# Kernel optimization log

Measured on AMD Instinct MI355X. Metric: run time of the kernel, lower is better.

The kernel has to match this reference:

```python
import jax, jax.numpy as jnp
import numpy as np

S, B, H, V = 64, 8, 512, 8192  # seq_length, batch, hidden, vocab
NEG = -1e9  # finite stand-in for -inf so gradients stay clean


def setup_inputs() -> dict:
    key = jax.random.key(0)
    ks = jax.random.split(key, 8)
    lin = lambda k, fi, fo: jax.random.normal(k, (fi, fo), jnp.float32) * 0.05
    return dict(
        h=jax.random.normal(ks[0], (S, B, H), jnp.float32) * 0.1,
        sentence=jax.random.randint(ks[1], (S, B), 0, V),
        t_W1=lin(ks[2], 2 * H, H), t_b1=jnp.zeros((H,), jnp.float32),
        t_W2=lin(ks[3], H, 1), t_b2=jnp.zeros((1,), jnp.float32),
        w_W1=lin(ks[4], 2 * H, H), w_b1=jnp.zeros((H,), jnp.float32),
        w_W2=lin(ks[5], H, V), w_b2=jnp.zeros((V,), jnp.float32),
    )


def _inside(h, sentence, t_W1, t_b1, t_W2, t_b2, w_W1, w_b1, w_W2, w_b2):
    sent_length = S - 1
    # ---- transition scores on full (i, j) grid: concat(h_i, h_j) -> MLP -> scalar
    hi = jnp.broadcast_to(h[:, None], (S, S, B, H))
    hj = jnp.broadcast_to(h[None, :], (S, S, B, H))
    feat = jnp.concatenate([hi, hj], axis=-1)                      # [S,S,B,2H]
    t = (jax.nn.relu(feat @ t_W1 + t_b1) @ t_W2 + t_b2)[..., 0]    # [S,S,B]
    sh_lp = jax.nn.log_sigmoid(-t)   # log p(shift | i, j)
    re_lp = jax.nn.log_sigmoid(t)    # log p(reduce | i, j)

    # ---- word generation log-probs for pairs (i, j), i < j <= sent_length-1
    iu, ju = jnp.triu_indices(sent_length, k=1)                    # P pairs
    hp = jnp.concatenate([h[iu], h[ju]], axis=-1)                  # [P,B,2H]
    logits = jax.nn.relu(hp @ w_W1 + w_b1) @ w_W2 + w_b2           # [P,B,V]
    lse = jax.scipy.special.logsumexp(logits, axis=-1)             # [P,B]
    tok = sentence[ju + 1]                                         # [P,B]
    tok_logit = jnp.take_along_axis(logits, tok[..., None], axis=-1)[..., 0]
    word_lp = tok_logit - lse
    # shift prob + word prob (word_prob_list in the original)
    wp = jnp.full((S, S, B), NEG, jnp.float32).at[iu, ju].set(sh_lp[iu, ju] + word_lp)

    # ---- DP table init
    table = jnp.full((S, S, B), NEG, jnp.float32)
    f0 = jnp.concatenate([h[0], h[0]], axis=-1)                    # [B,2H]
    lg0 = jax.nn.relu(f0 @ w_W1 + w_b1) @ w_W2 + w_b2              # [B,V]
    init_lp = jnp.take_along_axis(jax.nn.log_softmax(lg0, axis=-1),
                                  sentence[1][:, None], axis=1)[:, 0]
    table = table.at[0, 1].set(init_lp)
    jd = jnp.arange(1, sent_length)
    table = table.at[jd, jd + 1].set(0.0)

    # ---- diagonal sweep: table[i,j] = LSE_k( table[i,k]+table[k,j]+wp[i,k]+re[k,j] )
    ivec = jnp.arange(S)
    mvec = jnp.arange(1, S)

    def step(tab, g):
        i = ivec[:, None]
        m = mvec[None, :]
        k = jnp.clip(i + m, 0, S - 1)                              # [S,S-1]
        jv = jnp.clip(ivec + g, 0, S - 1)                          # [S]
        j = jv[:, None]
        valid = (m < g) & (ivec[:, None] + g <= sent_length)       # [S,S-1]
        sc = tab[i, k] + tab[k, j] + wp[i, k] + re_lp[k, j]        # [S,S-1,B]
        sc = jnp.where(valid[..., None], sc, NEG)
        mmax = jnp.max(sc, axis=1, keepdims=True)
        new = jnp.log(jnp.sum(jnp.exp(sc - mmax), axis=1)) + mmax[:, 0]
        row_ok = (ivec + g <= sent_length)[:, None]
        tab = tab.at[ivec, jv].set(jnp.where(row_ok, new, tab[ivec, jv]))
        return tab, None

    table, _ = jax.lax.scan(step, table, jnp.arange(2, sent_length + 1))
    final = table[0, sent_length] + re_lp[0, sent_length]          # [B]
    return -jnp.sum(final)  # neg_log_likelihood


def reference(h, sentence, t_W1, t_b1, t_W2, t_b2, w_W1, w_b1, w_W2, w_b2):
    return _inside(h, sentence, t_W1, t_b1, t_W2, t_b2, w_W1, w_b1, w_W2, w_b2)
```

## Files before the change

kernel.cpp:

```cpp
#include <hip/hip_runtime.h>
#include <hip/hip_bf16.h>
#include <hip/hip_fp8.h>
#include <math.h>

#define NEG (-1.0e9f)

typedef __bf16 bf16_t;
typedef __bf16 bf16x4 __attribute__((ext_vector_type(4)));
typedef __bf16 bf16x8 __attribute__((ext_vector_type(8)));
typedef float f32x4 __attribute__((ext_vector_type(4)));
typedef long i64x2 __attribute__((ext_vector_type(2)));
typedef unsigned char u8;
typedef unsigned long long u64;

#define SS 64
#define BB 8
#define HH 512
#define VV 8192
#define NPAIR 1953
#define NPTOT 1954
#define MROWS (NPTOT*BB)
#define MPAD  16384

__device__ __forceinline__ float logsig(float x) {
  return fminf(x, 0.f) - __logf(1.f + __expf(-fabsf(x)));
}
__device__ __forceinline__ u8 f2q(float x) { __hip_fp8_e4m3 q(x); return q.__x; }
__device__ __forceinline__ float q2f(u8 b) { __hip_fp8_e4m3 q; q.__x = b; return (float)q; }
__device__ __forceinline__ int ksl(int c) { return 2 * (c & 3) + (c >> 2); }

__global__ __launch_bounds__(256) void k_prep(
    const float* __restrict__ h,   bf16_t* __restrict__ hbf,
    const float* __restrict__ tW1, bf16_t* __restrict__ tW1T,
    const float* __restrict__ wW1, bf16_t* __restrict__ wW1T,
    const float* __restrict__ wW2, u8* __restrict__ w2t8) {
  __shared__ float tile[32][33];
  int blk = blockIdx.x, tid = threadIdx.x;
  if (blk < 256) {
    int gi = blk * 256 + tid;
    float4 v = ((const float4*)h)[gi];
    bf16x4 o = {(bf16_t)v.x, (bf16_t)v.y, (bf16_t)v.z, (bf16_t)v.w};
    ((bf16x4*)hbf)[gi] = o;
    return;
  }
  if (blk < 1280) {
    const float* in; bf16_t* out; int R = 1024, C = 512, t;
    if (blk < 768) { in = tW1; out = tW1T; t = blk - 256; }
    else           { in = wW1; out = wW1T; t = blk - 768; }
    int xt = C / 32;
    int c0 = (t % xt) * 32, r0 = (t / xt) * 32;
    int tx = tid & 31, ty = tid >> 5;
    for (int i = ty; i < 32; i += 8)
      tile[i][tx] = in[(size_t)(r0 + i) * C + c0 + tx];
    __syncthreads();
    for (int i = ty; i < 32; i += 8)
      out[(size_t)(c0 + i) * R + r0 + tx] = (bf16_t)tile[tx][i];
    return;
  }
  int t = blk - 1280;
  int c0 = (t % 256) * 32, r0 = (t / 256) * 32;
  int tx = tid & 31, ty = tid >> 5;
  for (int i = ty; i < 32; i += 8)
    tile[i][tx] = wW2[(size_t)(r0 + i) * 8192 + c0 + tx];
  __syncthreads();
  for (int i = ty; i < 32; i += 8) {
    int k = r0 + tx;
    int pos = (k >> 6) * 64 + ksl((k >> 3) & 7) * 8 + (k & 7);
    w2t8[(size_t)(c0 + i) * 512 + pos] = f2q(tile[tx][i]);
  }
}

__global__ __launch_bounds__(256) void k_gemm4(
    const bf16_t* __restrict__ A,
    const bf16_t* __restrict__ tW1T, const bf16_t* __restrict__ wW1T,
    float* __restrict__ Ut, float* __restrict__ Vt,
    float* __restrict__ Uw, float* __restrict__ Vw)
{
  __shared__ __align__(16) bf16_t As[128 * 32];
  __shared__ __align__(16) bf16_t Bs[128 * 32];
  const int tid = threadIdx.x;
  const int lane = tid & 63;
  const int wave = tid >> 6;
  const int wr = wave >> 1, wc = wave & 1;
  const int sel = blockIdx.x >> 4, sub = blockIdx.x & 15;
  const bf16_t* BT = (sel < 2 ? tW1T : wW1T) + (sel & 1) * 512;
  float* Cout = (sel == 0) ? Ut : (sel == 1) ? Vt : (sel == 2) ? Uw : Vw;
  const int m0 = (sub & 3) * 128, n0 = (sub >> 2) * 128;
  const int lda = 512, ldb = 1024, ldc = 512;

  const int rowS = tid >> 2;
  const int kS = (tid & 3) * 8;
  const bf16_t* gA0 = A + (size_t)(m0 + rowS) * lda + kS;
  const bf16_t* gA1 = A + (size_t)(m0 + rowS + 64) * lda + kS;
  const bf16_t* gB0 = BT + (size_t)(n0 + rowS) * ldb + kS;
  const bf16_t* gB1 = BT + (size_t)(n0 + rowS + 64) * ldb + kS;

  f32x4 acc[4][4] = {};
  const int aoff = (wr * 64 + (lane & 15)) * 32 + (lane >> 4) * 8;
  const int boff = (wc * 64 + (lane & 15)) * 32 + (lane >> 4) * 8;

  for (int k0 = 0; k0 < 512; k0 += 32) {
    __builtin_amdgcn_global_load_lds((const __attribute__((address_space(1))) void*)(gA0 + k0),
        (__attribute__((address_space(3))) void*)(As + wave * 512), 16, 0, 0);
    __builtin_amdgcn_global_load_lds((const __attribute__((address_space(1))) void*)(gA1 + k0),
        (__attribute__((address_space(3))) void*)(As + 2048 + wave * 512), 16, 0, 0);
    __builtin_amdgcn_global_load_lds((const __attribute__((address_space(1))) void*)(gB0 + k0),
        (__attribute__((address_space(3))) void*)(Bs + wave * 512), 16, 0, 0);
    __builtin_amdgcn_global_load_lds((const __attribute__((address_space(1))) void*)(gB1 + k0),
        (__attribute__((address_space(3))) void*)(Bs + 2048 + wave * 512), 16, 0, 0);
    __syncthreads();
    bf16x8 af[4], bfr[4];
    #pragma unroll
    for (int mf = 0; mf < 4; ++mf) af[mf] = *(const bf16x8*)&As[aoff + mf * 16 * 32];
    #pragma unroll
    for (int nf = 0; nf < 4; ++nf) bfr[nf] = *(const bf16x8*)&Bs[boff + nf * 16 * 32];
    #pragma unroll
    for (int mf = 0; mf < 4; ++mf)
      #pragma unroll
      for (int nf = 0; nf < 4; ++nf)
        acc[mf][nf] = __builtin_amdgcn_mfma_f32_16x16x32_bf16(af[mf], bfr[nf], acc[mf][nf], 0, 0, 0);
    __syncthreads();
  }
  #pragma unroll
  for (int mf = 0; mf < 4; ++mf)
    #pragma unroll
    for (int r2 = 0; r2 < 4; ++r2) {
      int grow = m0 + wr * 64 + mf * 16 + (lane >> 4) * 4 + r2;
      #pragma unroll
      for (int nf = 0; nf < 4; ++nf) {
        int gcol = n0 + wc * 64 + nf * 16 + (lane & 15);
        Cout[(size_t)grow * ldc + gcol] = acc[mf][nf][r2];
      }
    }
}

#define STAGEA(b, h, kt) do { \
  const u8* _s = A8 + (size_t)(m0 + (h)*128 + (tid>>2)) * 512 + (kt)*64 + csrc; \
  __builtin_amdgcn_global_load_lds((const __attribute__((address_space(1))) void*)_s, \
    (__attribute__((address_space(3))) void*)(As + (b)*16384 + (h)*8192 + (tid>>6)*1024), 16, 0, 0); \
} while(0)

#define STAGEB(b, h, kt) do { \
  const u8* _s = BT8 + (size_t)(n0 + (h)*128 + (tid>>2)) * 512 + (kt)*64 + csrc; \
  __builtin_amdgcn_global_load_lds((const __attribute__((address_space(1))) void*)_s, \
    (__attribute__((address_space(3))) void*)(Bs + (b)*16384 + (h)*8192 + (tid>>6)*1024), 16, 0, 0); \
} while(0)

#define LDA(b, mh) do { \
  _Pragma("unroll") \
  for (int _m = 0; _m < 4; ++_m) \
    afv[_m] = *(const i64x2*)(As + (b)*16384 + (mh)*8192 + ardE + _m*1024); \
} while(0)

#define LDB(b, nh) do { \
  _Pragma("unroll") \
  for (int _n = 0; _n < 2; ++_n) \
    bfv[nh][_n] = *(const i64x2*)(Bs + (b)*16384 + (nh)*8192 + brdE + _n*1024); \
} while(0)

#define MMA(mh, nh) do { \
  __builtin_amdgcn_s_setprio(1); \
  _Pragma("unroll") \
  for (int _m = 0; _m < 4; ++_m) \
    _Pragma("unroll") \
    for (int _n = 0; _n < 2; ++_n) { \
      acc[(mh)*4+_m][(nh)*2+_n] = __builtin_amdgcn_mfma_f32_16x16x32_fp8_fp8( \
          afv[_m][0], bfv[nh][_n][0], acc[(mh)*4+_m][(nh)*2+_n], 0, 0, 0); \
      acc[(mh)*4+_m][(nh)*2+_n] = __builtin_amdgcn_mfma_f32_16x16x32_fp8_fp8( \
          afv[_m][1], bfv[nh][_n][1], acc[(mh)*4+_m][(nh)*2+_n], 0, 0, 0); \
    } \
  __builtin_amdgcn_s_setprio(0); \
} while(0)

#define BARLG() do { __builtin_amdgcn_s_barrier(); \
  asm volatile("s_waitcnt lgkmcnt(0)" ::: "memory"); \
  __builtin_amdgcn_sched_barrier(0); } while(0)
#define ENDPH() __builtin_amdgcn_s_barrier()
#define CKPT() asm volatile("s_waitcnt vmcnt(2)" ::: "memory")

__global__ __launch_bounds__(512, 2) void k_gemm256(
    const u8* __restrict__ A8,
    const u8* __restrict__ BT8,
    const float* __restrict__ bias,
    float* __restrict__ sumexp)
{
  __shared__ __align__(16) u8 As[2 * 16384];
  __shared__ __align__(16) u8 Bs[2 * 16384];
  const int tid = threadIdx.x;
  const int l = tid & 63;
  const int wave = tid >> 6;
  const int wr = wave >> 2, wc = wave & 3;

  const int xcd = blockIdx.x & 7, sub = blockIdx.x >> 3;
  const int mt = xcd * 8 + (sub & 7);
  const int nt = sub >> 3;
  const int m0 = mt * 256, n0 = nt * 256;

  const int csrc = (((tid & 3) ^ ((tid >> 3) & 3)) << 4);
  const int rsw = (((l >> 4) ^ ((l & 15) >> 1)) & 3) << 4;
  const int ardE = (wr * 64 + (l & 15)) * 64 + rsw;
  const int brdE = (wc * 32 + (l & 15)) * 64 + rsw;

  f32x4 acc[8][4] = {};
  i64x2 afv[4];
  i64x2 bfv[2][2];

  STAGEA(0, 0, 0); STAGEA(0, 1, 0); STAGEB(0, 0, 0); STAGEB(0, 1, 0);
  STAGEA(1, 0, 1); STAGEB(1, 0, 1);
  CKPT();
  __builtin_amdgcn_s_barrier();

  #pragma unroll 1
  for (int t = 0; t < 4; ++t) {
    int tA = 2 * t + 1;
    int tB = 2 * t + 2; if (tB > 7) tB = 7;
    int tC = 2 * t + 3; if (tC > 7) tC = 7;
    LDA(0, 0); LDB(0, 0); STAGEA(1, 1, tA); BARLG(); MMA(0, 0); ENDPH();
    LDB(0, 1);            STAGEB(1, 1, tA); BARLG(); MMA(0, 1); ENDPH();
    LDA(0, 1);            STAGEA(0, 0, tB); BARLG(); MMA(1, 0); ENDPH();
                          STAGEB(0, 0, tB); BARLG(); MMA(1, 1); CKPT(); ENDPH();
    LDA(1, 0); LDB(1, 0); STAGEA(0, 1, tB); BARLG(); MMA(0, 0); ENDPH();
    LDB(1, 1);            STAGEB(0, 1, tB); BARLG(); MMA(0, 1); ENDPH();
    LDA(1, 1);            STAGEA(1, 0, tC); BARLG(); MMA(1, 0); ENDPH();
                          STAGEB(1, 0, tC); BARLG(); MMA(1, 1); CKPT(); ENDPH();
  }

  float b2v[4];
  #pragma unroll
  for (int nf = 0; nf < 4; ++nf)
    b2v[nf] = bias[n0 + (nf >> 1) * 128 + wc * 32 + (nf & 1) * 16 + (l & 15)];
  #pragma unroll
  for (int mf = 0; mf < 8; ++mf) {
    #pragma unroll
    for (int r2 = 0; r2 < 4; ++r2) {
      float s = 0.f;
      #pragma unroll
      for (int nf = 0; nf < 4; ++nf)
        s += __expf(acc[mf][nf][r2] + b2v[nf]);
      s += __shfl_xor(s, 1); s += __shfl_xor(s, 2);
      s += __shfl_xor(s, 4); s += __shfl_xor(s, 8);
      if ((l & 15) == 0)
        atomicAdd(&sumexp[m0 + (mf >> 2) * 128 + wr * 64 + (mf & 3) * 16 + (l >> 4) * 4 + r2], s);
    }
  }
}

__global__ __launch_bounds__(256) void k_actnet(
    const float* __restrict__ Uw, const float* __restrict__ Vw,
    const float* __restrict__ wb1, u8* __restrict__ act8,
    float* __restrict__ sumexp,
    const u8* __restrict__ w2t8, const int* __restrict__ sent,
    const float* __restrict__ wb2, float* __restrict__ tok_logit,
    const float* __restrict__ Ut, const float* __restrict__ Vt,
    const float* __restrict__ tb1, const float* __restrict__ tW2,
    const float* __restrict__ tb2,
    float* __restrict__ sh_lp, float* __restrict__ re_lp)
{
  __shared__ float pd[512];
  if (blockIdx.x < 2048) {
    int p = blockIdx.x;
    if (threadIdx.x < 8) sumexp[p * 8 + threadIdx.x] = 0.f;
    int iu = 0, ju = 0;
    bool real = (p < NPTOT);
    if (p < NPAIR) {
      int i = 0, base = 0;
      while (base + (62 - i) <= p) { base += 62 - i; ++i; }
      iu = i; ju = i + 1 + (p - base);
    }
    const int srow = (p < NPAIR) ? (ju + 1) : 1;
    for (int t = threadIdx.x; t < 512; t += 256) {
      int b = t >> 6, c = t & 63;
      int wpos = (c >> 3) * 64 + ksl(c & 7) * 8;
      u64 bytes = 0;
      if (real) {
        const float4* u4 = (const float4*)(Uw + (size_t)(iu * BB + b) * HH);
        const float4* v4 = (const float4*)(Vw + (size_t)(ju * BB + b) * HH);
        const float4* bb4 = (const float4*)wb1;
        #pragma unroll
        for (int q = 0; q < 2; ++q) {
          float4 uu = u4[c * 2 + q], vv = v4[c * 2 + q], bb = bb4[c * 2 + q];
          bytes |= (u64)f2q(fmaxf(uu.x + vv.x + bb.x, 0.f)) << (8 * (q * 4 + 0));
          bytes |= (u64)f2q(fmaxf(uu.y + vv.y + bb.y, 0.f)) << (8 * (q * 4 + 1));
          bytes |= (u64)f2q(fmaxf(uu.z + vv.z + bb.z, 0.f)) << (8 * (q * 4 + 2));
          bytes |= (u64)f2q(fmaxf(uu.w + vv.w + bb.w, 0.f)) << (8 * (q * 4 + 3));
        }
      }
      *(u64*)(act8 + (size_t)(p * 8 + b) * 512 + wpos) = bytes;
      float s = 0.f;
      if (real) {
        int tok = sent[srow * BB + b];
        u64 wv = *(const u64*)(w2t8 + (size_t)tok * 512 + wpos);
        #pragma unroll
        for (int e = 0; e < 8; ++e)
          s += q2f((u8)(bytes >> (8 * e))) * q2f((u8)(wv >> (8 * e)));
      }
      pd[t] = s;
    }
    __syncthreads();
    if (real) {
      int wv_ = threadIdx.x >> 6, ln = threadIdx.x & 63;
      #pragma unroll
      for (int rr = 0; rr < 2; ++rr) {
        int b = wv_ * 2 + rr;
        float s = pd[b * 64 + ln];
        #pragma unroll
        for (int off = 1; off < 64; off <<= 1) s += __shfl_xor(s, off);
        if (ln == 0) {
          int tok = sent[srow * BB + b];
          tok_logit[p * 8 + b] = s + wb2[tok];
        }
      }
    }
    return;
  }
  int gid = (blockIdx.x - 2048) * 4 + (threadIdx.x >> 6);
  int lane = threadIdx.x & 63;
  int b = gid & 7, j = (gid >> 3) & 63, i = gid >> 9;
  const float4* u = (const float4*)(Ut + (size_t)(i * BB + b) * HH);
  const float4* v = (const float4*)(Vt + (size_t)(j * BB + b) * HH);
  const float4* bb = (const float4*)tb1;
  const float4* ww = (const float4*)tW2;
  float s = 0.f;
  #pragma unroll
  for (int qq = 0; qq < 2; ++qq) {
    int c = lane * 2 + qq;
    float4 uu = u[c], vv = v[c], b4 = bb[c], w4 = ww[c];
    s += fmaxf(uu.x + vv.x + b4.x, 0.f) * w4.x;
    s += fmaxf(uu.y + vv.y + b4.y, 0.f) * w4.y;
    s += fmaxf(uu.z + vv.z + b4.z, 0.f) * w4.z;
    s += fmaxf(uu.w + vv.w + b4.w, 0.f) * w4.w;
  }
  #pragma unroll
  for (int off = 1; off < 64; off <<= 1) s += __shfl_xor(s, off);
  if (lane == 0) {
    float t = s + tb2[0];
    re_lp[gid] = logsig(t);
    sh_lp[gid] = logsig(-t);
  }
}

__global__ __launch_bounds__(1024) void k_dp(const float* __restrict__ sh_lp, const float* __restrict__ re_lp,
                                             const float* __restrict__ tok_logit, const float* __restrict__ sumexp,
                                             float* __restrict__ finals) {
  int b = blockIdx.x;
  __shared__ float tab[4096];
  __shared__ float wpl[4096];
  __shared__ float rel[4096];
  int tid = threadIdx.x;
  for (int idx = tid; idx < 4096; idx += 1024) {
    tab[idx] = NEG;
    int i = idx >> 6, j = idx & 63;
    float w = NEG;
    if (i < j && j <= 62) {
      int p = i * 62 - i * (i - 1) / 2 + (j - i - 1);
      int r = p * 8 + b;
      w = sh_lp[idx * 8 + b] + (tok_logit[r] - __logf(sumexp[r]));
    }
    wpl[idx] = w;
    rel[idx] = re_lp[idx * 8 + b];
  }
  __syncthreads();
  if (tid == 0) tab[1] = tok_logit[NPAIR * 8 + b] - __logf(sumexp[NPAIR * 8 + b]);
  if (tid >= 1 && tid <= 62) tab[tid * 64 + tid + 1] = 0.f;
  __syncthreads();
  int lane = tid & 63, wave = tid >> 6;
  for (int g = 2; g <= 63; ++g) {
    int cnt = 64 - g;
    if (g <= 17) {
      int seg = lane >> 4, sl = lane & 15;
      int i = wave * 4 + seg;
      if (i < cnt) {
        int m = sl + 1;
        int j = i + g, k = i + m;
        float sc = NEG;
        if (m < g) sc = tab[i * 64 + k] + tab[k * 64 + j] + wpl[i * 64 + k] + rel[k * 64 + j];
        float mx = sc;
        #pragma unroll
        for (int off = 1; off < 16; off <<= 1) mx = fmaxf(mx, __shfl_xor(mx, off));
        float e = (m < g) ? __expf(sc - mx) : 0.f;
        #pragma unroll
        for (int off = 1; off < 16; off <<= 1) e += __shfl_xor(e, off);
        if (sl == 0) tab[i * 64 + j] = __logf(e) + mx;
      }
    } else {
      for (int i = wave; i < cnt; i += 16) {
        int m = lane + 1;
        int j = i + g, k = i + m;
        float sc = NEG;
        if (m < g) sc = tab[i * 64 + k] + tab[k * 64 + j] + wpl[i * 64 + k] + rel[k * 64 + j];
        float mx = sc;
        #pragma unroll
        for (int off = 1; off < 64; off <<= 1) mx = fmaxf(mx, __shfl_xor(mx, off));
        float e = (m < g) ? __expf(sc - mx) : 0.f;
        #pragma unroll
        for (int off = 1; off < 64; off <<= 1) e += __shfl_xor(e, off);
        if (lane == 0) tab[i * 64 + j] = __logf(e) + mx;
      }
    }
    __syncthreads();
  }
  if (tid == 0) finals[b] = tab[63] + rel[63];
}

__global__ void k_final(const float* __restrict__ finals, float* __restrict__ out) {
  if (threadIdx.x == 0) {
    float s = 0.f;
    for (int b = 0; b < 8; ++b) s += finals[b];
    out[0] = -s;
  }
}

extern "C" void kernel_launch(void* const* d_in, const int* in_sizes, int n_in,
                              void* d_out, int out_size, void* d_ws, size_t ws_size,
                              hipStream_t stream) {
  const float* h    = (const float*)d_in[0];
  const int*   sent = (const int*)d_in[1];
  const float* tW1  = (const float*)d_in[2];
  const float* tb1  = (const float*)d_in[3];
  const float* tW2  = (const float*)d_in[4];
  const float* tb2  = (const float*)d_in[5];
  const float* wW1  = (const float*)d_in[6];
  const float* wb1  = (const float*)d_in[7];
  const float* wW2  = (const float*)d_in[8];
  const float* wb2  = (const float*)d_in[9];
  float* out = (float*)d_out;

  char* ws = (char*)d_ws;
  size_t off = 0;
  auto alloc = [&](size_t bytes) { char* p = ws + off; off += (bytes + 255) & ~(size_t)255; return p; };
  bf16_t* hbf    = (bf16_t*)alloc((size_t)512 * 512 * 2);
  bf16_t* tW1T   = (bf16_t*)alloc((size_t)512 * 1024 * 2);
  bf16_t* wW1T   = (bf16_t*)alloc((size_t)512 * 1024 * 2);
  u8*     w2t8   = (u8*)alloc((size_t)VV * HH);
  float*  Ut     = (float*)alloc((size_t)512 * 512 * 4);
  float*  Vt     = (float*)alloc((size_t)512 * 512 * 4);
  float*  Uw     = (float*)alloc((size_t)512 * 512 * 4);
  float*  Vw     = (float*)alloc((size_t)512 * 512 * 4);
  u8*     act8   = (u8*)alloc((size_t)MPAD * HH);
  float*  sumexp = (float*)alloc((size_t)MPAD * 4);
  float*  tokl   = (float*)alloc((size_t)MPAD * 4);
  float*  shlp   = (float*)alloc((size_t)32768 * 4);
  float*  relp   = (float*)alloc((size_t)32768 * 4);
  float*  finals = (float*)alloc(256);

  k_prep<<<5376, 256, 0, stream>>>(h, hbf, tW1, tW1T, wW1, wW1T, wW2, w2t8);
  k_gemm4<<<64, 256, 0, stream>>>(hbf, tW1T, wW1T, Ut, Vt, Uw, Vw);
  k_actnet<<<2048 + 8192, 256, 0, stream>>>(Uw, Vw, wb1, act8, sumexp, w2t8, sent, wb2, tokl,
                                            Ut, Vt, tb1, tW2, tb2, shlp, relp);
  k_gemm256<<<2048, 512, 0, stream>>>(act8, w2t8, wb2, sumexp);
  k_dp<<<8, 1024, 0, stream>>>(shlp, relp, tokl, sumexp, finals);
  k_final<<<1, 64, 0, stream>>>(finals, out);
}
```

Baseline: 288.2 us.

## Tile transition MLP over 8x8 pair blocks, move W2 quantize into small GEMM launch

```diff
diff --git a/kernel.cpp b/kernel.cpp
--- a/kernel.cpp
+++ b/kernel.cpp
@@ -32,8 +32,7 @@
 __global__ __launch_bounds__(256) void k_prep(
     const float* __restrict__ h,   bf16_t* __restrict__ hbf,
     const float* __restrict__ tW1, bf16_t* __restrict__ tW1T,
-    const float* __restrict__ wW1, bf16_t* __restrict__ wW1T,
-    const float* __restrict__ wW2, u8* __restrict__ w2t8) {
+    const float* __restrict__ wW1, bf16_t* __restrict__ wW1T) {
   __shared__ float tile[32][33];
   int blk = blockIdx.x, tid = threadIdx.x;
   if (blk < 256) {
@@ -43,42 +42,45 @@
     ((bf16x4*)hbf)[gi] = o;
     return;
   }
-  if (blk < 1280) {
-    const float* in; bf16_t* out; int R = 1024, C = 512, t;
-    if (blk < 768) { in = tW1; out = tW1T; t = blk - 256; }
-    else           { in = wW1; out = wW1T; t = blk - 768; }
-    int xt = C / 32;
-    int c0 = (t % xt) * 32, r0 = (t / xt) * 32;
-    int tx = tid & 31, ty = tid >> 5;
-    for (int i = ty; i < 32; i += 8)
-      tile[i][tx] = in[(size_t)(r0 + i) * C + c0 + tx];
-    __syncthreads();
-    for (int i = ty; i < 32; i += 8)
-      out[(size_t)(c0 + i) * R + r0 + tx] = (bf16_t)tile[tx][i];
-    return;
-  }
-  int t = blk - 1280;
-  int c0 = (t % 256) * 32, r0 = (t / 256) * 32;
+  const float* in; bf16_t* out; int R = 1024, C = 512, t;
+  if (blk < 768) { in = tW1; out = tW1T; t = blk - 256; }
+  else           { in = wW1; out = wW1T; t = blk - 768; }
+  int xt = C / 32;
+  int c0 = (t % xt) * 32, r0 = (t / xt) * 32;
   int tx = tid & 31, ty = tid >> 5;
   for (int i = ty; i < 32; i += 8)
-    tile[i][tx] = wW2[(size_t)(r0 + i) * 8192 + c0 + tx];
+    tile[i][tx] = in[(size_t)(r0 + i) * C + c0 + tx];
   __syncthreads();
-  for (int i = ty; i < 32; i += 8) {
-    int k = r0 + tx;
-    int pos = (k >> 6) * 64 + ksl((k >> 3) & 7) * 8 + (k & 7);
-    w2t8[(size_t)(c0 + i) * 512 + pos] = f2q(tile[tx][i]);
-  }
-}
-
-__global__ __launch_bounds__(256) void k_gemm4(
+  for (int i = ty; i < 32; i += 8)
+    out[(size_t)(c0 + i) * R + r0 + tx] = (bf16_t)tile[tx][i];
+}
+
+__global__ __launch_bounds__(256) void k_gemm4t(
     const bf16_t* __restrict__ A,
     const bf16_t* __restrict__ tW1T, const bf16_t* __restrict__ wW1T,
     float* __restrict__ Ut, float* __restrict__ Vt,
-    float* __restrict__ Uw, float* __restrict__ Vw)
+    float* __restrict__ Uw, float* __restrict__ Vw,
+    const float* __restrict__ wW2, u8* __restrict__ w2t8)
 {
-  __shared__ __align__(16) bf16_t As[128 * 32];
-  __shared__ __align__(16) bf16_t Bs[128 * 32];
+  __shared__ __align__(16) char lds_raw[16384];
   const int tid = threadIdx.x;
+  if (blockIdx.x >= 64) {
+    float* tile = (float*)lds_raw;
+    int t = blockIdx.x - 64;
+    int c0 = (t % 256) * 32, r0 = (t / 256) * 32;
+    int tx = tid & 31, ty = tid >> 5;
+    for (int i = ty; i < 32; i += 8)
+      tile[i * 33 + tx] = wW2[(size_t)(r0 + i) * 8192 + c0 + tx];
+    __syncthreads();
+    for (int i = ty; i < 32; i += 8) {
+      int k = r0 + tx;
+      int pos = (k >> 6) * 64 + ksl((k >> 3) & 7) * 8 + (k & 7);
+      w2t8[(size_t)(c0 + i) * 512 + pos] = f2q(tile[tx * 33 + i]);
+    }
+    return;
+  }
+  bf16_t* As = (bf16_t*)lds_raw;
+  bf16_t* Bs = (bf16_t*)(lds_raw + 8192);
   const int lane = tid & 63;
   const int wave = tid >> 6;
   const int wr = wave >> 1, wc = wave & 1;
@@ -215,14 +217,14 @@
     int tA = 2 * t + 1;
     int tB = 2 * t + 2; if (tB > 7) tB = 7;
     int tC = 2 * t + 3; if (tC > 7) tC = 7;
-    LDA(0, 0); LDB(0, 0); STAGEA(1, 1, tA); BARLG(); MMA(0, 0); ENDPH();
-    LDB(0, 1);            STAGEB(1, 1, tA); BARLG(); MMA(0, 1); ENDPH();
-    LDA(0, 1);            STAGEA(0, 0, tB); BARLG(); MMA(1, 0); ENDPH();
-                          STAGEB(0, 0, tB); BARLG(); MMA(1, 1); CKPT(); ENDPH();
-    LDA(1, 0); LDB(1, 0); STAGEA(0, 1, tB); BARLG(); MMA(0, 0); ENDPH();
-    LDB(1, 1);            STAGEB(0, 1, tB); BARLG(); MMA(0, 1); ENDPH();
-    LDA(1, 1);            STAGEA(1, 0, tC); BARLG(); MMA(1, 0); ENDPH();
-                          STAGEB(1, 0, tC); BARLG(); MMA(1, 1); CKPT(); ENDPH();
+    LDA(0, 0); LDB(0, 0); LDB(0, 1); STAGEA(1, 1, tA); STAGEB(1, 1, tA);
+      BARLG(); MMA(0, 0); MMA(0, 1); ENDPH();
+    LDA(0, 1);                       STAGEA(0, 0, tB); STAGEB(0, 0, tB);
+      BARLG(); MMA(1, 0); MMA(1, 1); CKPT(); ENDPH();
+    LDA(1, 0); LDB(1, 0); LDB(1, 1); STAGEA(0, 1, tB); STAGEB(0, 1, tB);
+      BARLG(); MMA(0, 0); MMA(0, 1); ENDPH();
+    LDA(1, 1);                       STAGEA(1, 0, tC); STAGEB(1, 0, tC);
+      BARLG(); MMA(1, 0); MMA(1, 1); CKPT(); ENDPH();
   }
 
   float b2v[4];
@@ -256,8 +258,9 @@
     const float* __restrict__ tb2,
     float* __restrict__ sh_lp, float* __restrict__ re_lp)
 {
-  __shared__ float pd[512];
+  __shared__ float ldsf[8192];
   if (blockIdx.x < 2048) {
+    float* pd = ldsf;
     int p = blockIdx.x;
     if (threadIdx.x < 8) sumexp[p * 8 + threadIdx.x] = 0.f;
     int iu = 0, ju = 0;
@@ -313,29 +316,37 @@
     }
     return;
   }
-  int gid = (blockIdx.x - 2048) * 4 + (threadIdx.x >> 6);
-  int lane = threadIdx.x & 63;
-  int b = gid & 7, j = (gid >> 3) & 63, i = gid >> 9;
-  const float4* u = (const float4*)(Ut + (size_t)(i * BB + b) * HH);
-  const float4* v = (const float4*)(Vt + (size_t)(j * BB + b) * HH);
-  const float4* bb = (const float4*)tb1;
-  const float4* ww = (const float4*)tW2;
-  float s = 0.f;
+  int t = blockIdx.x - 2048;
+  int b = t & 7, pr = t >> 3;
+  int ig = 0, base = 0;
+  while (base + (8 - ig) <= pr) { base += 8 - ig; ++ig; }
+  int jg = ig + (pr - base);
+  float* Us = ldsf;
+  float* Vs = ldsf + 4096;
+  for (int q = threadIdx.x; q < 1024; q += 256) {
+    int ii = q >> 7, cc = q & 127;
+    ((float4*)Us)[ii * 128 + cc] = ((const float4*)(Ut + (size_t)((ig * 8 + ii) * BB + b) * HH))[cc];
+    ((float4*)Vs)[ii * 128 + cc] = ((const float4*)(Vt + (size_t)((jg * 8 + ii) * BB + b) * HH))[cc];
+  }
+  __syncthreads();
+  int lane = threadIdx.x & 63, wv_ = threadIdx.x >> 6;
+  float b1r[8], w2r[8];
   #pragma unroll
-  for (int qq = 0; qq < 2; ++qq) {
-    int c = lane * 2 + qq;
-    float4 uu = u[c], vv = v[c], b4 = bb[c], w4 = ww[c];
-    s += fmaxf(uu.x + vv.x + b4.x, 0.f) * w4.x;
-    s += fmaxf(uu.y + vv.y + b4.y, 0.f) * w4.y;
-    s += fmaxf(uu.z + vv.z + b4.z, 0.f) * w4.z;
-    s += fmaxf(uu.w + vv.w + b4.w, 0.f) * w4.w;
-  }
-  #pragma unroll
-  for (int off = 1; off < 64; off <<= 1) s += __shfl_xor(s, off);
-  if (lane == 0) {
-    float t = s + tb2[0];
-    re_lp[gid] = logsig(t);
-    sh_lp[gid] = logsig(-t);
+  for (int k = 0; k < 8; ++k) { b1r[k] = tb1[lane + 64 * k]; w2r[k] = tW2[lane + 64 * k]; }
+  for (int pp = wv_; pp < 64; pp += 4) {
+    int ii = pp >> 3, jj = pp & 7;
+    int i = ig * 8 + ii, j = jg * 8 + jj;
+    float s = 0.f;
+    #pragma unroll
+    for (int k = 0; k < 8; ++k)
+      s += fmaxf(Us[ii * 512 + lane + 64 * k] + Vs[jj * 512 + lane + 64 * k] + b1r[k], 0.f) * w2r[k];
+    #pragma unroll
+    for (int off = 1; off < 64; off <<= 1) s += __shfl_xor(s, off);
+    if (lane == 0 && i < j) {
+      float tv = s + tb2[0];
+      re_lp[(i * 64 + j) * 8 + b] = logsig(tv);
+      sh_lp[(i * 64 + j) * 8 + b] = logsig(-tv);
+    }
   }
 }
 
@@ -357,7 +368,7 @@
       w = sh_lp[idx * 8 + b] + (tok_logit[r] - __logf(sumexp[r]));
     }
     wpl[idx] = w;
-    rel[idx] = re_lp[idx * 8 + b];
+    rel[idx] = (idx >> 6) < (idx & 63) ? re_lp[idx * 8 + b] : NEG;
   }
   __syncthreads();
   if (tid == 0) tab[1] = tok_logit[NPAIR * 8 + b] - __logf(sumexp[NPAIR * 8 + b]);
@@ -443,10 +454,10 @@
   float*  relp   = (float*)alloc((size_t)32768 * 4);
   float*  finals = (float*)alloc(256);
 
-  k_prep<<<5376, 256, 0, stream>>>(h, hbf, tW1, tW1T, wW1, wW1T, wW2, w2t8);
-  k_gemm4<<<64, 256, 0, stream>>>(hbf, tW1T, wW1T, Ut, Vt, Uw, Vw);
-  k_actnet<<<2048 + 8192, 256, 0, stream>>>(Uw, Vw, wb1, act8, sumexp, w2t8, sent, wb2, tokl,
-                                            Ut, Vt, tb1, tW2, tb2, shlp, relp);
+  k_prep<<<1280, 256, 0, stream>>>(h, hbf, tW1, tW1T, wW1, wW1T);
+  k_gemm4t<<<4160, 256, 0, stream>>>(hbf, tW1T, wW1T, Ut, Vt, Uw, Vw, wW2, w2t8);
+  k_actnet<<<2048 + 288, 256, 0, stream>>>(Uw, Vw, wb1, act8, sumexp, w2t8, sent, wb2, tokl,
+                                           Ut, Vt, tb1, tW2, tb2, shlp, relp);
   k_gemm256<<<2048, 512, 0, stream>>>(act8, w2t8, wb2, sumexp);
   k_dp<<<8, 1024, 0, stream>>>(shlp, relp, tokl, sumexp, finals);
   k_final<<<1, 64, 0, stream>>>(finals, out);
```

After: 288.9 us. Within noise of the previous version (+0.3%).
